# Kernel optimization log

Hardware: AMD Instinct MI355X
Metric: run time of the kernel (lower is better)

## Reference

```python
import jax, jax.numpy as jnp
import numpy as np

B, T, D_IN = 256, 250, 700
H1, H2, D_OUT = 256, 256, 20
B_J0 = 0.01
BETA = 1.8  # adaptation strength (isAdapt=1)
LENS, SCALE, HIGHT, GAMMA = 0.5, 6.0, 0.15, 0.5
SQRT_2PI = float(np.sqrt(2.0 * np.pi))


def _gaussian(x, mu, sigma):
    return jnp.exp(-((x - mu) ** 2) / (2.0 * sigma ** 2)) / (SQRT_2PI * sigma)


@jax.custom_vjp
def act_fun(x):
    # Heaviside spike with multi-Gaussian surrogate gradient (gradient_type='MG')
    return (x > 0).astype(x.dtype)


def _act_fwd(x):
    return act_fun(x), x


def _act_bwd(x, g):
    temp = (_gaussian(x, 0.0, LENS) * (1.0 + HIGHT)
            - _gaussian(x, LENS, SCALE * LENS) * HIGHT
            - _gaussian(x, -LENS, SCALE * LENS) * HIGHT)
    return (g * temp * GAMMA,)


act_fun.defvjp(_act_fwd, _act_bwd)


def setup_inputs() -> dict:
    key = jax.random.key(0)
    ks = jax.random.split(key, 16)
    # binary-ish spike input (SHD spike trains), rand fill
    x = (jax.random.uniform(ks[0], (B, T, D_IN)) < 0.1).astype(jnp.float32)

    def xavier(k, out_d, in_d):
        lim = float(np.sqrt(6.0 / (in_d + out_d)))
        return jax.random.uniform(k, (out_d, in_d), jnp.float32, -lim, lim)

    return {
        "x": x,
        "w_i2h1": xavier(ks[1], H1, D_IN),
        "w_h12h1": xavier(ks[2], H1, H1),
        "w_h12h2": xavier(ks[3], H2, H1),
        "w_h22h2": xavier(ks[4], H2, H2),
        "w_h2o": xavier(ks[5], D_OUT, H2),
        "b_h1": jnp.zeros((H1,), jnp.float32),
        "b_h2": jnp.zeros((H2,), jnp.float32),
        "b_o": jnp.zeros((D_OUT,), jnp.float32),
        "tau_adp_h1": 150.0 + 10.0 * jax.random.normal(ks[6], (H1,), jnp.float32),
        "tau_adp_h2": 150.0 + 10.0 * jax.random.normal(ks[7], (H2,), jnp.float32),
        "tau_m_h1": 20.0 + 5.0 * jax.random.normal(ks[8], (H1,), jnp.float32),
        "tau_m_h2": 20.0 + 5.0 * jax.random.normal(ks[9], (H2,), jnp.float32),
        "tau_m_o": 20.0 + 5.0 * jax.random.normal(ks[10], (D_OUT,), jnp.float32),
    }


def _lif_step(inp, mem, spk, b, alpha, ro):
    # mem_update_adp with params=None, dparams=None, isAdapt=1, dt=1, R_m=1
    b = ro * b + BETA * (1.0 - ro) * spk
    mem = mem * alpha - b * spk + (1.0 - alpha) * inp
    spk = act_fun(mem - b - B_J0)
    return mem, spk, b


def reference(x, w_i2h1, w_h12h1, w_h12h2, w_h22h2, w_h2o,
              b_h1, b_h2, b_o, tau_adp_h1, tau_adp_h2,
              tau_m_h1, tau_m_h2, tau_m_o):
    bsz = x.shape[0]
    h1, h2, d_out = w_i2h1.shape[0], w_h12h2.shape[0], w_h2o.shape[0]

    alpha1 = jnp.exp(-1.0 / tau_m_h1)
    ro1 = jnp.exp(-1.0 / tau_adp_h1)
    alpha2 = jnp.exp(-1.0 / tau_m_h2)
    ro2 = jnp.exp(-1.0 / tau_adp_h2)
    alpha_o = jnp.exp(-1.0 / tau_m_o)

    init = (
        jnp.zeros((bsz, h1)), jnp.zeros((bsz, h1)), jnp.full((bsz, h1), B_J0),
        jnp.zeros((bsz, h2)), jnp.zeros((bsz, h2)), jnp.full((bsz, h2), B_J0),
        jnp.zeros((bsz, d_out)), jnp.zeros((bsz, d_out)),
    )
    xT = jnp.swapaxes(x, 0, 1)  # [T, B, D_in]

    def step(carry, xt):
        mem1, spk1, bb1, mem2, spk2, bb2, mem_o, acc = carry
        h1_in = xt @ w_i2h1.T + spk1 @ w_h12h1.T + b_h1
        mem1, spk1, bb1 = _lif_step(h1_in, mem1, spk1, bb1, alpha1, ro1)
        h2_in = spk1 @ w_h12h2.T + spk2 @ w_h22h2.T + b_h2
        mem2, spk2, bb2 = _lif_step(h2_in, mem2, spk2, bb2, alpha2, ro2)
        o_in = spk2 @ w_h2o.T + b_o
        mem_o = mem_o * alpha_o + (1.0 - alpha_o) * o_in  # output_Neuron
        acc = acc + jax.nn.softmax(mem_o, axis=-1)
        return (mem1, spk1, bb1, mem2, spk2, bb2, mem_o, acc), None

    carry, _ = jax.lax.scan(step, init, xT)
    return carry[-1]  # accumulated softmax over the 250 timesteps, [B, 20]
```

## Files before the change

kernel.cpp:

```cpp
#include <hip/hip_runtime.h>
#include <cstdint>
#include <cstddef>

#define BB 256
#define TT 250
#define DIN 700
#define H1 256
#define H2 256
#define DOUT 20
#define BJ0 0.01f
#define BETAC 1.8f
#define DUMMY 256
#define IQSCALE 3.814697265625e-06f

typedef float f32x4 __attribute__((ext_vector_type(4)));
typedef short s16x4 __attribute__((ext_vector_type(4)));
typedef int   i32x4 __attribute__((ext_vector_type(4)));

#define COFF_BL  180224
#define IOFF_P12 90112
#define SOFF_T22 311808
#define FOFF_W2O 188800
#define FOFF_XP  193944
#define FOFF_MO  16577944
#define N_TRANS  316948

#define BARRIER_LDS() asm volatile("s_waitcnt lgkmcnt(0)\n\ts_barrier" ::: "memory")

__device__ __forceinline__ short q18(float w) {
    float s = w * 262144.0f;
    s = fminf(fmaxf(s, -32767.0f), 32767.0f);
    return (short)__float2int_rn(s);
}

__global__ void transpose_all_k(const float* __restrict__ w_i2h1,
                                const float* __restrict__ w_h12h1,
                                const float* __restrict__ w_h12h2,
                                const float* __restrict__ w_h22h2,
                                const float* __restrict__ w_h2o,
                                signed char* __restrict__ cws,
                                short* __restrict__ sws,
                                int* __restrict__ iws,
                                float* __restrict__ fws) {
    int i = blockIdx.x * blockDim.x + threadIdx.x;
    if (i < 180224) {
        int h = i / 704, k = i - h * 704;
        int q = (k < DIN) ? (int)q18(w_i2h1[h * DIN + k]) : 0;
        q = q > 32639 ? 32639 : (q < -32640 ? -32640 : q);
        int hi = (q + 128) >> 8;
        int lo = q - (hi << 8);
        cws[i] = (signed char)hi;
        cws[COFF_BL + i] = (signed char)lo;
        return;
    }
    i -= 180224;
    if (i < 65792) { int d = i >> 8, h = i & 255;
        unsigned int lo = 0, hi = 0;
        if (d < H1) {
            lo = (unsigned short)q18(w_h12h1[h * H1 + d]);
            hi = (unsigned short)q18(w_h12h2[h * H1 + d]);
        }
        iws[IOFF_P12 + i] = (int)(lo | (hi << 16)); return; }
    i -= 65792;
    if (i < 65792) { int d = i >> 8, h = i & 255;
        sws[SOFF_T22 + i] = q18((d < H2) ? w_h22h2[h * H2 + d] : 0.f); return; }
    i -= 65792;
    if (i < 5140)  { int j = i / 20, h = i % 20;
        fws[FOFF_W2O + i] = (j < H2) ? w_h2o[h * H2 + j] : 0.f; return; }
}

__global__ __launch_bounds__(256) void xgemm_k(const float* __restrict__ x,
                                               const signed char* __restrict__ Bh,
                                               const signed char* __restrict__ Bl,
                                               const float* __restrict__ b_h1,
                                               float* __restrict__ Xp) {
    const int t    = threadIdx.x;
    const int lane = t & 63;
    const int w    = t >> 6;
    const int m0   = blockIdx.x * 32;

    __shared__ __align__(16) signed char Asub[32 * 720];
    __shared__ __align__(16) signed char Bhs[256 * 80];
    __shared__ __align__(16) signed char Bls[256 * 80];

    #pragma unroll
    for (int it = 0; it < 22; ++it) {
        int flat = it * 256 + t;
        int row  = flat / 176;
        int c4   = flat - row * 176;
        unsigned int pk = 0u;
        if (c4 < 175) {
            const float* xr = x + (size_t)(m0 + row) * DIN;
            float4 f = *(const float4*)(xr + (c4 << 2));
            pk = (f.x != 0.f ? 1u : 0u)
               | (f.y != 0.f ? 1u : 0u) << 8
               | (f.z != 0.f ? 1u : 0u) << 16
               | (f.w != 0.f ? 1u : 0u) << 24;
        }
        *(unsigned int*)(Asub + row * 720 + (c4 << 2)) = pk;
    }

    i32x4 acch[2][4], accl[2][4];
    #pragma unroll
    for (int mt = 0; mt < 2; ++mt)
        #pragma unroll
        for (int nt = 0; nt < 4; ++nt) {
            acch[mt][nt] = (i32x4){0, 0, 0, 0};
            accl[mt][nt] = (i32x4){0, 0, 0, 0};
        }

    const int arow  = lane & 15;
    const int kg16  = (lane >> 4) << 4;
    const int bcol0 = w << 6;

    for (int ks = 0; ks < 11; ++ks) {
        __syncthreads();
        #pragma unroll
        for (int it2 = 0; it2 < 4; ++it2) {
            int row = it2 * 64 + (t >> 2);
            int ch  = (t & 3) << 4;
            int go  = row * 704 + ks * 64 + ch;
            *(int4*)(Bhs + row * 80 + ch) = *(const int4*)(Bh + go);
            *(int4*)(Bls + row * 80 + ch) = *(const int4*)(Bl + go);
        }
        __syncthreads();

        const int ko = ks * 64 + kg16;
        i32x4 a0 = *(const i32x4*)(Asub + arow * 720 + ko);
        i32x4 a1 = *(const i32x4*)(Asub + (16 + arow) * 720 + ko);
        #pragma unroll
        for (int nt = 0; nt < 4; ++nt) {
            const int bb = (bcol0 + nt * 16 + arow) * 80 + kg16;
            i32x4 bhf = *(const i32x4*)(Bhs + bb);
            i32x4 blf = *(const i32x4*)(Bls + bb);
            acch[0][nt] = __builtin_amdgcn_mfma_i32_16x16x64_i8(a0, bhf, acch[0][nt], 0, 0, 0);
            acch[1][nt] = __builtin_amdgcn_mfma_i32_16x16x64_i8(a1, bhf, acch[1][nt], 0, 0, 0);
            accl[0][nt] = __builtin_amdgcn_mfma_i32_16x16x64_i8(a0, blf, accl[0][nt], 0, 0, 0);
            accl[1][nt] = __builtin_amdgcn_mfma_i32_16x16x64_i8(a1, blf, accl[1][nt], 0, 0, 0);
        }
    }

    const int crb = (lane >> 4) << 2;
    #pragma unroll
    for (int nt = 0; nt < 4; ++nt) {
        int col = bcol0 + nt * 16 + arow;
        float bias = b_h1[col];
        #pragma unroll
        for (int mt = 0; mt < 2; ++mt) {
            #pragma unroll
            for (int r = 0; r < 4; ++r) {
                int row = m0 + mt * 16 + crb + r;
                int ir = (acch[mt][nt][r] << 8) + accl[mt][nt][r];
                __builtin_nontemporal_store(bias + (float)ir * IQSCALE,
                                            Xp + (size_t)row * H1 + col);
            }
        }
    }
}

__global__ __launch_bounds__(512) void rec_k(
    const float* __restrict__ Xp,
    const int*   __restrict__ sP12,
    const short* __restrict__ sT22, const float* __restrict__ wT2o,
    const float* __restrict__ b_h2, const float* __restrict__ b_o,
    const float* __restrict__ tau_adp_h1, const float* __restrict__ tau_adp_h2,
    const float* __restrict__ tau_m_h1, const float* __restrict__ tau_m_h2,
    const float* __restrict__ tau_m_o,
    float* __restrict__ Mo) {
    const int tid  = threadIdx.x;
    const int h    = tid & 255;
    const int half = tid >> 8;
    const int lane = tid & 63;
    const int g    = tid >> 6;
    const int l4   = lane << 2;
    const int b    = blockIdx.x;
    const float* __restrict__ XpB = Xp + (size_t)b * TT * H1;
    float* __restrict__ MoB = Mo + (size_t)b * TT * DOUT;

    __shared__ __align__(16) short sT22L[65792];
    __shared__ __align__(16) int lst1s[2][256];
    __shared__ __align__(16) int lst2s[2][256];
    __shared__ __align__(16) int lcnt[2][2];
    __shared__ __align__(16) int pp11[8][256];
    __shared__ __align__(16) int pp12[8][256];
    __shared__ __align__(16) int pp22[8][256];
    __shared__ __align__(16) float pro[8][20];

    {
        const int* src = (const int*)sT22;
        int* dst = (int*)sT22L;
        for (int i2 = tid; i2 < 32896; i2 += 512) dst[i2] = src[i2];
        if (tid < 4) lcnt[tid >> 1][tid & 1] = 0;
    }

    const float alpha1 = expf(-1.0f / tau_m_h1[h]);
    const float ro1    = expf(-1.0f / tau_adp_h1[h]);
    const float alpha2 = expf(-1.0f / tau_m_h2[h]);
    const float ro2    = expf(-1.0f / tau_adp_h2[h]);
    const float bh2v   = b_h2[h];
    float alpo = 0.f, bov = 0.f;
    if (h < DOUT) { alpo = expf(-1.0f / tau_m_o[h]); bov = b_o[h]; }

    float mem1 = 0.f, spk1 = 0.f, bb1v = BJ0;
    float mem2 = 0.f, spk2 = 0.f, bb2v = BJ0;
    float memo = 0.f;

    float xp_cur = 0.f;
    if (half == 0) xp_cur = __builtin_nontemporal_load(XpB + h);
    __syncthreads();

    for (int i = 0; i <= TT + 1; ++i) {
        const int cur = i & 1, nxt = cur ^ 1;

        float xp_nxt = 0.f;
        if (half == 0 && i + 1 < TT)
            xp_nxt = __builtin_nontemporal_load(XpB + (size_t)(i + 1) * H1 + h);

        const int tot1 = lcnt[cur][0];
        const int tot2 = lcnt[cur][1];
        const int n1p = (tot1 + 31) & ~31;
        const int n2p = (tot2 + 31) & ~31;

        if (half == 0) lst1s[nxt][h] = DUMMY; else lst2s[nxt][h] = DUMMY;
        if (tid == 0)   lcnt[nxt][0] = 0;
        if (tid == 256) lcnt[nxt][1] = 0;

        int a110 = 0, a111 = 0, a112 = 0, a113 = 0;
        int a120 = 0, a121 = 0, a122 = 0, a123 = 0;
        int a220 = 0, a221 = 0, a222 = 0, a223 = 0;
        float ao0 = 0.f, ao1 = 0.f, ao2 = 0.f, ao3 = 0.f;

        const int gbase = g << 5;
        const int ng1 = n1p >> 3;
        for (int kk = 0; kk < ng1; kk += 4) {
            int4 e = *(const int4*)&lst1s[cur][gbase + kk];
            int4 pa = *(const int4*)(sP12 + ((size_t)e.x << 8) + l4);
            int4 pb = *(const int4*)(sP12 + ((size_t)e.y << 8) + l4);
            int4 pc = *(const int4*)(sP12 + ((size_t)e.z << 8) + l4);
            int4 pd = *(const int4*)(sP12 + ((size_t)e.w << 8) + l4);
            a110 += ((int)(short)pa.x + (int)(short)pb.x) + ((int)(short)pc.x + (int)(short)pd.x);
            a111 += ((int)(short)pa.y + (int)(short)pb.y) + ((int)(short)pc.y + (int)(short)pd.y);
            a112 += ((int)(short)pa.z + (int)(short)pb.z) + ((int)(short)pc.z + (int)(short)pd.z);
            a113 += ((int)(short)pa.w + (int)(short)pb.w) + ((int)(short)pc.w + (int)(short)pd.w);
            a120 += ((pa.x >> 16) + (pb.x >> 16)) + ((pc.x >> 16) + (pd.x >> 16));
            a121 += ((pa.y >> 16) + (pb.y >> 16)) + ((pc.y >> 16) + (pd.y >> 16));
            a122 += ((pa.z >> 16) + (pb.z >> 16)) + ((pc.z >> 16) + (pd.z >> 16));
            a123 += ((pa.w >> 16) + (pb.w >> 16)) + ((pc.w >> 16) + (pd.w >> 16));
        }
        const int ng2 = n2p >> 3;
        for (int kk = 0; kk < ng2; kk += 4) {
            int4 e = *(const int4*)&lst2s[cur][gbase + kk];
            s16x4 wa = *(const s16x4*)(sT22L + (e.x << 8) + l4);
            s16x4 wb = *(const s16x4*)(sT22L + (e.y << 8) + l4);
            s16x4 wc = *(const s16x4*)(sT22L + (e.z << 8) + l4);
            s16x4 wd = *(const s16x4*)(sT22L + (e.w << 8) + l4);
            a220 += (wa.x + wb.x) + (wc.x + wd.x);
            a221 += (wa.y + wb.y) + (wc.y + wd.y);
            a222 += (wa.z + wb.z) + (wc.z + wd.z);
            a223 += (wa.w + wb.w) + (wc.w + wd.w);
            if (lane < 5) {
                float4 va = *(const float4*)(wT2o + e.x * DOUT + l4);
                float4 vb = *(const float4*)(wT2o + e.y * DOUT + l4);
                float4 vc = *(const float4*)(wT2o + e.z * DOUT + l4);
                float4 vd = *(const float4*)(wT2o + e.w * DOUT + l4);
                ao0 += (va.x + vb.x) + (vc.x + vd.x);
                ao1 += (va.y + vb.y) + (vc.y + vd.y);
                ao2 += (va.z + vb.z) + (vc.z + vd.z);
                ao3 += (va.w + vb.w) + (vc.w + vd.w);
            }
        }
        {
            int4 v;
            v.x = a110; v.y = a111; v.z = a112; v.w = a113;
            *(int4*)&pp11[g][l4] = v;
            v.x = a120; v.y = a121; v.z = a122; v.w = a123;
            *(int4*)&pp12[g][l4] = v;
            v.x = a220; v.y = a221; v.z = a222; v.w = a223;
            *(int4*)&pp22[g][l4] = v;
        }
        if (lane < 5) {
            float4 v; v.x = ao0; v.y = ao1; v.z = ao2; v.w = ao3;
            *(float4*)&pro[g][l4] = v;
        }
        BARRIER_LDS();

        if (half == 0) {
            if (i < TT) {
                int ir11 = ((pp11[0][h] + pp11[1][h]) + (pp11[2][h] + pp11[3][h]))
                         + ((pp11[4][h] + pp11[5][h]) + (pp11[6][h] + pp11[7][h]));
                float r1 = (float)ir11 * IQSCALE;
                bb1v = ro1 * bb1v + BETAC * (1.f - ro1) * spk1;
                mem1 = mem1 * alpha1 - bb1v * spk1 + (1.f - alpha1) * (xp_cur + r1);
                float ns1 = (mem1 - bb1v - BJ0) > 0.f ? 1.f : 0.f;
                spk1 = ns1;
                unsigned long long m1 = __ballot(ns1 != 0.f ? 1 : 0);
                int c = __popcll(m1);
                int base = 0;
                if (lane == 0) base = atomicAdd(&lcnt[nxt][0], c);
                base = __shfl(base, 0);
                if (ns1 != 0.f) {
                    int pos = base + __popcll(m1 & ((1ull << lane) - 1ull));
                    lst1s[nxt][((pos & 7) << 5) + (pos >> 3)] = h;
                }
            }
        } else {
            if (i >= 1 && i <= TT) {
                int ir12 = ((pp12[0][h] + pp12[1][h]) + (pp12[2][h] + pp12[3][h]))
                         + ((pp12[4][h] + pp12[5][h]) + (pp12[6][h] + pp12[7][h]));
                int ir22 = ((pp22[0][h] + pp22[1][h]) + (pp22[2][h] + pp22[3][h]))
                         + ((pp22[4][h] + pp22[5][h]) + (pp22[6][h] + pp22[7][h]));
                float r23 = (float)(ir22 + ir12) * IQSCALE;
                bb2v = ro2 * bb2v + BETAC * (1.f - ro2) * spk2;
                mem2 = mem2 * alpha2 - bb2v * spk2 + (1.f - alpha2) * (bh2v + r23);
                float ns2 = (mem2 - bb2v - BJ0) > 0.f ? 1.f : 0.f;
                spk2 = ns2;
                unsigned long long m2 = __ballot(ns2 != 0.f ? 1 : 0);
                int c = __popcll(m2);
                int base = 0;
                if (lane == 0) base = atomicAdd(&lcnt[nxt][1], c);
                base = __shfl(base, 0);
                if (ns2 != 0.f) {
                    int pos = base + __popcll(m2 & ((1ull << lane) - 1ull));
                    lst2s[nxt][((pos & 7) << 5) + (pos >> 3)] = h;
                }
            }
            if ((h < DOUT) && (i >= 2)) {
                float ro = ((pro[0][h] + pro[1][h]) + (pro[2][h] + pro[3][h]))
                         + ((pro[4][h] + pro[5][h]) + (pro[6][h] + pro[7][h]));
                memo = memo * alpo + (1.f - alpo) * (bov + ro);
                __builtin_nontemporal_store(memo, MoB + (size_t)(i - 2) * DOUT + h);
            }
        }
        BARRIER_LDS();

        xp_cur = xp_nxt;
    }
}

__global__ __launch_bounds__(256) void soft_k(const float* __restrict__ Mo,
                                              float* __restrict__ out) {
    const int b = blockIdx.x;
    const int t = threadIdx.x;
    __shared__ float sm[TT][DOUT];

    if (t < TT) {
        const float* row = Mo + ((size_t)b * TT + t) * DOUT;
        float v[DOUT];
        #pragma unroll
        for (int k = 0; k < DOUT; k += 4) {
            float4 r = *(const float4*)(row + k);
            v[k] = r.x; v[k + 1] = r.y; v[k + 2] = r.z; v[k + 3] = r.w;
        }
        float mx = v[0];
        #pragma unroll
        for (int j = 1; j < DOUT; ++j) mx = fmaxf(mx, v[j]);
        float s = 0.f;
        #pragma unroll
        for (int j = 0; j < DOUT; ++j) { v[j] = __expf(v[j] - mx); s += v[j]; }
        float inv = 1.0f / s;
        #pragma unroll
        for (int j = 0; j < DOUT; ++j) sm[t][j] = v[j] * inv;
    }
    __syncthreads();
    if (t < DOUT) {
        float acc = 0.f;
        for (int tt = 0; tt < TT; ++tt) acc += sm[tt][t];
        out[b * DOUT + t] = acc;
    }
}

extern "C" void kernel_launch(void* const* d_in, const int* in_sizes, int n_in,
                              void* d_out, int out_size, void* d_ws, size_t ws_size,
                              hipStream_t stream) {
    const float* x          = (const float*)d_in[0];
    const float* w_i2h1     = (const float*)d_in[1];
    const float* w_h12h1    = (const float*)d_in[2];
    const float* w_h12h2    = (const float*)d_in[3];
    const float* w_h22h2    = (const float*)d_in[4];
    const float* w_h2o      = (const float*)d_in[5];
    const float* b_h1       = (const float*)d_in[6];
    const float* b_h2       = (const float*)d_in[7];
    const float* b_o        = (const float*)d_in[8];
    const float* tau_adp_h1 = (const float*)d_in[9];
    const float* tau_adp_h2 = (const float*)d_in[10];
    const float* tau_m_h1   = (const float*)d_in[11];
    const float* tau_m_h2   = (const float*)d_in[12];
    const float* tau_m_o    = (const float*)d_in[13];

    signed char* cws = (signed char*)d_ws;
    short* sws = (short*)d_ws;
    int*   iws = (int*)d_ws;
    float* fws = (float*)d_ws;
    const signed char* Bh = cws;
    const signed char* Bl = cws + COFF_BL;
    const int*   sP12 = iws + IOFF_P12;
    const short* sT22 = sws + SOFF_T22;
    float* wT2o = fws + FOFF_W2O;
    float* Xp   = fws + FOFF_XP;
    float* Mo   = fws + FOFF_MO;

    transpose_all_k<<<(N_TRANS + 255) / 256, 256, 0, stream>>>(
        w_i2h1, w_h12h1, w_h12h2, w_h22h2, w_h2o, cws, sws, iws, fws);

    xgemm_k<<<(BB * TT) / 32, 256, 0, stream>>>(x, Bh, Bl, b_h1, Xp);

    rec_k<<<BB, 512, 0, stream>>>(Xp, sP12, sT22, wT2o,
                                  b_h2, b_o, tau_adp_h1, tau_adp_h2,
                                  tau_m_h1, tau_m_h2, tau_m_o, Mo);

    soft_k<<<BB, 256, 0, stream>>>(Mo, (float*)d_out);
}
```

Before: 753.8 us.

## Assign layer-1 and layer-2 neurons to separate waves with one barrier per step

Restructures the recurrent kernel so waves 0-3 own layer-1 neurons and waves 4-7 own layer-2 neurons. Each thread gathers its own column over the full spike list, instead of splitting the spike list across waves and reducing partial sums through shared memory. This removes the partial-sum arrays and one of the two barriers per timestep. The spike-count slots are now rotated over four entries, and the output weights are staged in LDS. In exchange each thread does serial gathers over the whole spike list, which lengthens the per-step critical path when many neurons spike. The split layer-1/layer-2 weight arrays also use scalar 16-bit gathers from global memory rather than packed vector loads.

Measured after the change: 689.6 us. -8.5%, faster.

```diff
diff --git a/kernel.cpp b/kernel.cpp
--- a/kernel.cpp
+++ b/kernel.cpp
@@ -10,20 +10,19 @@
 #define DOUT 20
 #define BJ0 0.01f
 #define BETAC 1.8f
-#define DUMMY 256
 #define IQSCALE 3.814697265625e-06f
 
 typedef float f32x4 __attribute__((ext_vector_type(4)));
-typedef short s16x4 __attribute__((ext_vector_type(4)));
 typedef int   i32x4 __attribute__((ext_vector_type(4)));
 
 #define COFF_BL  180224
-#define IOFF_P12 90112
-#define SOFF_T22 311808
-#define FOFF_W2O 188800
-#define FOFF_XP  193944
-#define FOFF_MO  16577944
-#define N_TRANS  316948
+#define SOFF_T11 180224
+#define SOFF_T12 245760
+#define SOFF_T22 311296
+#define FOFF_W2O 188416
+#define FOFF_XP  193536
+#define FOFF_MO  16577536
+#define N_TRANS  381952
 
 #define BARRIER_LDS() asm volatile("s_waitcnt lgkmcnt(0)\n\ts_barrier" ::: "memory")
 
@@ -40,7 +39,6 @@
                                 const float* __restrict__ w_h2o,
                                 signed char* __restrict__ cws,
                                 short* __restrict__ sws,
-                                int* __restrict__ iws,
                                 float* __restrict__ fws) {
     int i = blockIdx.x * blockDim.x + threadIdx.x;
     if (i < 180224) {
@@ -54,19 +52,17 @@
         return;
     }
     i -= 180224;
-    if (i < 65792) { int d = i >> 8, h = i & 255;
-        unsigned int lo = 0, hi = 0;
-        if (d < H1) {
-            lo = (unsigned short)q18(w_h12h1[h * H1 + d]);
-            hi = (unsigned short)q18(w_h12h2[h * H1 + d]);
-        }
-        iws[IOFF_P12 + i] = (int)(lo | (hi << 16)); return; }
-    i -= 65792;
-    if (i < 65792) { int d = i >> 8, h = i & 255;
-        sws[SOFF_T22 + i] = q18((d < H2) ? w_h22h2[h * H2 + d] : 0.f); return; }
-    i -= 65792;
-    if (i < 5140)  { int j = i / 20, h = i % 20;
-        fws[FOFF_W2O + i] = (j < H2) ? w_h2o[h * H2 + j] : 0.f; return; }
+    if (i < 65536) { int d = i >> 8, h = i & 255;
+        sws[SOFF_T11 + i] = q18(w_h12h1[h * H1 + d]); return; }
+    i -= 65536;
+    if (i < 65536) { int d = i >> 8, h = i & 255;
+        sws[SOFF_T12 + i] = q18(w_h12h2[h * H1 + d]); return; }
+    i -= 65536;
+    if (i < 65536) { int d = i >> 8, h = i & 255;
+        sws[SOFF_T22 + i] = q18(w_h22h2[h * H2 + d]); return; }
+    i -= 65536;
+    if (i < 5120)  { int j = i / 20, o = i % 20;
+        fws[FOFF_W2O + i] = w_h2o[o * H2 + j]; return; }
 }
 
 __global__ __launch_bounds__(256) void xgemm_k(const float* __restrict__ x,
@@ -160,7 +156,7 @@
 
 __global__ __launch_bounds__(512) void rec_k(
     const float* __restrict__ Xp,
-    const int*   __restrict__ sP12,
+    const short* __restrict__ sT11, const short* __restrict__ sT12,
     const short* __restrict__ sT22, const float* __restrict__ wT2o,
     const float* __restrict__ b_h2, const float* __restrict__ b_o,
     const float* __restrict__ tau_adp_h1, const float* __restrict__ tau_adp_h2,
@@ -168,171 +164,168 @@
     const float* __restrict__ tau_m_o,
     float* __restrict__ Mo) {
     const int tid  = threadIdx.x;
-    const int h    = tid & 255;
-    const int half = tid >> 8;
     const int lane = tid & 63;
-    const int g    = tid >> 6;
-    const int l4   = lane << 2;
+    const int w    = tid >> 6;
+    const bool isL1 = (w < 4);
+    const int c    = ((w & 3) << 6) + lane;
     const int b    = blockIdx.x;
     const float* __restrict__ XpB = Xp + (size_t)b * TT * H1;
     float* __restrict__ MoB = Mo + (size_t)b * TT * DOUT;
 
-    __shared__ __align__(16) short sT22L[65792];
+    __shared__ __align__(16) short sT22L[65536];
+    __shared__ __align__(16) float w2oL[5120];
     __shared__ __align__(16) int lst1s[2][256];
     __shared__ __align__(16) int lst2s[2][256];
-    __shared__ __align__(16) int lcnt[2][2];
-    __shared__ __align__(16) int pp11[8][256];
-    __shared__ __align__(16) int pp12[8][256];
-    __shared__ __align__(16) int pp22[8][256];
-    __shared__ __align__(16) float pro[8][20];
+    __shared__ __align__(16) int lcnt[4][2];
 
     {
         const int* src = (const int*)sT22;
         int* dst = (int*)sT22L;
-        for (int i2 = tid; i2 < 32896; i2 += 512) dst[i2] = src[i2];
-        if (tid < 4) lcnt[tid >> 1][tid & 1] = 0;
-    }
-
-    const float alpha1 = expf(-1.0f / tau_m_h1[h]);
-    const float ro1    = expf(-1.0f / tau_adp_h1[h]);
-    const float alpha2 = expf(-1.0f / tau_m_h2[h]);
-    const float ro2    = expf(-1.0f / tau_adp_h2[h]);
-    const float bh2v   = b_h2[h];
+        for (int k = tid; k < 32768; k += 512) dst[k] = src[k];
+        for (int k = tid; k < 5120; k += 512) w2oL[k] = wT2o[k];
+        if (tid < 256) { lst1s[0][tid] = 0; lst1s[1][tid] = 0;
+                         lst2s[0][tid] = 0; lst2s[1][tid] = 0; }
+        if (tid < 8) ((int*)lcnt)[tid] = 0;
+    }
+
+    float alpha, rr, inb = 0.f;
+    if (isL1) {
+        alpha = expf(-1.0f / tau_m_h1[c]);
+        rr    = expf(-1.0f / tau_adp_h1[c]);
+    } else {
+        alpha = expf(-1.0f / tau_m_h2[c]);
+        rr    = expf(-1.0f / tau_adp_h2[c]);
+        inb   = b_h2[c];
+    }
+    const int oc  = ((w & 3) * 5) + lane;
+    const int ocs = (isL1 && lane < 5) ? oc : 0;
     float alpo = 0.f, bov = 0.f;
-    if (h < DOUT) { alpo = expf(-1.0f / tau_m_o[h]); bov = b_o[h]; }
-
-    float mem1 = 0.f, spk1 = 0.f, bb1v = BJ0;
-    float mem2 = 0.f, spk2 = 0.f, bb2v = BJ0;
+    if (isL1 && lane < 5) { alpo = expf(-1.0f / tau_m_o[oc]); bov = b_o[oc]; }
+
+    float mem = 0.f, spk = 0.f, bbv = BJ0;
     float memo = 0.f;
 
     float xp_cur = 0.f;
-    if (half == 0) xp_cur = __builtin_nontemporal_load(XpB + h);
+    if (isL1) xp_cur = __builtin_nontemporal_load(XpB + c);
     __syncthreads();
 
     for (int i = 0; i <= TT + 1; ++i) {
         const int cur = i & 1, nxt = cur ^ 1;
+        const int cc = i & 3, cn = (i + 1) & 3, cz = (i + 2) & 3;
+
+        const int tot1 = lcnt[cc][0];
+        const int tot2 = lcnt[cc][1];
+        if (tid == 0) { lcnt[cz][0] = 0; lcnt[cz][1] = 0; }
 
         float xp_nxt = 0.f;
-        if (half == 0 && i + 1 < TT)
-            xp_nxt = __builtin_nontemporal_load(XpB + (size_t)(i + 1) * H1 + h);
-
-        const int tot1 = lcnt[cur][0];
-        const int tot2 = lcnt[cur][1];
-        const int n1p = (tot1 + 31) & ~31;
-        const int n2p = (tot2 + 31) & ~31;
-
-        if (half == 0) lst1s[nxt][h] = DUMMY; else lst2s[nxt][h] = DUMMY;
-        if (tid == 0)   lcnt[nxt][0] = 0;
-        if (tid == 256) lcnt[nxt][1] = 0;
-
-        int a110 = 0, a111 = 0, a112 = 0, a113 = 0;
-        int a120 = 0, a121 = 0, a122 = 0, a123 = 0;
-        int a220 = 0, a221 = 0, a222 = 0, a223 = 0;
-        float ao0 = 0.f, ao1 = 0.f, ao2 = 0.f, ao3 = 0.f;
-
-        const int gbase = g << 5;
-        const int ng1 = n1p >> 3;
-        for (int kk = 0; kk < ng1; kk += 4) {
-            int4 e = *(const int4*)&lst1s[cur][gbase + kk];
-            int4 pa = *(const int4*)(sP12 + ((size_t)e.x << 8) + l4);
-            int4 pb = *(const int4*)(sP12 + ((size_t)e.y << 8) + l4);
-            int4 pc = *(const int4*)(sP12 + ((size_t)e.z << 8) + l4);
-            int4 pd = *(const int4*)(sP12 + ((size_t)e.w << 8) + l4);
-            a110 += ((int)(short)pa.x + (int)(short)pb.x) + ((int)(short)pc.x + (int)(short)pd.x);
-            a111 += ((int)(short)pa.y + (int)(short)pb.y) + ((int)(short)pc.y + (int)(short)pd.y);
-            a112 += ((int)(short)pa.z + (int)(short)pb.z) + ((int)(short)pc.z + (int)(short)pd.z);
-            a113 += ((int)(short)pa.w + (int)(short)pb.w) + ((int)(short)pc.w + (int)(short)pd.w);
-            a120 += ((pa.x >> 16) + (pb.x >> 16)) + ((pc.x >> 16) + (pd.x >> 16));
-            a121 += ((pa.y >> 16) + (pb.y >> 16)) + ((pc.y >> 16) + (pd.y >> 16));
-            a122 += ((pa.z >> 16) + (pb.z >> 16)) + ((pc.z >> 16) + (pd.z >> 16));
-            a123 += ((pa.w >> 16) + (pb.w >> 16)) + ((pc.w >> 16) + (pd.w >> 16));
-        }
-        const int ng2 = n2p >> 3;
-        for (int kk = 0; kk < ng2; kk += 4) {
-            int4 e = *(const int4*)&lst2s[cur][gbase + kk];
-            s16x4 wa = *(const s16x4*)(sT22L + (e.x << 8) + l4);
-            s16x4 wb = *(const s16x4*)(sT22L + (e.y << 8) + l4);
-            s16x4 wc = *(const s16x4*)(sT22L + (e.z << 8) + l4);
-            s16x4 wd = *(const s16x4*)(sT22L + (e.w << 8) + l4);
-            a220 += (wa.x + wb.x) + (wc.x + wd.x);
-            a221 += (wa.y + wb.y) + (wc.y + wd.y);
-            a222 += (wa.z + wb.z) + (wc.z + wd.z);
-            a223 += (wa.w + wb.w) + (wc.w + wd.w);
-            if (lane < 5) {
-                float4 va = *(const float4*)(wT2o + e.x * DOUT + l4);
-                float4 vb = *(const float4*)(wT2o + e.y * DOUT + l4);
-                float4 vc = *(const float4*)(wT2o + e.z * DOUT + l4);
-                float4 vd = *(const float4*)(wT2o + e.w * DOUT + l4);
-                ao0 += (va.x + vb.x) + (vc.x + vd.x);
-                ao1 += (va.y + vb.y) + (vc.y + vd.y);
-                ao2 += (va.z + vb.z) + (vc.z + vd.z);
-                ao3 += (va.w + vb.w) + (vc.w + vd.w);
-            }
-        }
-        {
-            int4 v;
-            v.x = a110; v.y = a111; v.z = a112; v.w = a113;
-            *(int4*)&pp11[g][l4] = v;
-            v.x = a120; v.y = a121; v.z = a122; v.w = a123;
-            *(int4*)&pp12[g][l4] = v;
-            v.x = a220; v.y = a221; v.z = a222; v.w = a223;
-            *(int4*)&pp22[g][l4] = v;
-        }
-        if (lane < 5) {
-            float4 v; v.x = ao0; v.y = ao1; v.z = ao2; v.w = ao3;
-            *(float4*)&pro[g][l4] = v;
-        }
+        if (isL1 && i + 1 < TT)
+            xp_nxt = __builtin_nontemporal_load(XpB + (size_t)(i + 1) * H1 + c);
+
+        const int* __restrict__ L1l = lst1s[cur];
+        const int* __restrict__ L2l = lst2s[cur];
+
+        int acc1 = 0, acc2 = 0;
+        float ao = 0.f;
+
+        if (isL1) {
+            if (i < TT) {
+                const short* colT = sT11 + c;
+                int nb = tot1 >> 2, rem = tot1 & 3;
+                for (int kk = 0; kk < nb; ++kk) {
+                    int4 e = *(const int4*)(L1l + (kk << 2));
+                    acc1 += colT[e.x << 8]; acc1 += colT[e.y << 8];
+                    acc1 += colT[e.z << 8]; acc1 += colT[e.w << 8];
+                }
+                if (rem) {
+                    int4 e = *(const int4*)(L1l + (nb << 2));
+                    acc1 += colT[e.x << 8];
+                    if (rem > 1) acc1 += colT[e.y << 8];
+                    if (rem > 2) acc1 += colT[e.z << 8];
+                }
+            }
+            if (i >= 2) {
+                int nb = tot2 >> 2, rem = tot2 & 3;
+                for (int kk = 0; kk < nb; ++kk) {
+                    int4 e = *(const int4*)(L2l + (kk << 2));
+                    float v0 = w2oL[e.x * DOUT + ocs];
+                    float v1 = w2oL[e.y * DOUT + ocs];
+                    float v2 = w2oL[e.z * DOUT + ocs];
+                    float v3 = w2oL[e.w * DOUT + ocs];
+                    ao += (v0 + v1) + (v2 + v3);
+                }
+                if (rem) {
+                    int4 e = *(const int4*)(L2l + (nb << 2));
+                    ao += w2oL[e.x * DOUT + ocs];
+                    if (rem > 1) ao += w2oL[e.y * DOUT + ocs];
+                    if (rem > 2) ao += w2oL[e.z * DOUT + ocs];
+                }
+            }
+        } else if (i >= 1 && i <= TT) {
+            {
+                const short* colT = sT12 + c;
+                int nb = tot1 >> 2, rem = tot1 & 3;
+                for (int kk = 0; kk < nb; ++kk) {
+                    int4 e = *(const int4*)(L1l + (kk << 2));
+                    acc1 += colT[e.x << 8]; acc1 += colT[e.y << 8];
+                    acc1 += colT[e.z << 8]; acc1 += colT[e.w << 8];
+                }
+                if (rem) {
+                    int4 e = *(const int4*)(L1l + (nb << 2));
+                    acc1 += colT[e.x << 8];
+                    if (rem > 1) acc1 += colT[e.y << 8];
+                    if (rem > 2) acc1 += colT[e.z << 8];
+                }
+            }
+            {
+                const short* colL = sT22L + c;
+                int nb = tot2 >> 2, rem = tot2 & 3;
+                for (int kk = 0; kk < nb; ++kk) {
+                    int4 e = *(const int4*)(L2l + (kk << 2));
+                    acc2 += colL[e.x << 8]; acc2 += colL[e.y << 8];
+                    acc2 += colL[e.z << 8]; acc2 += colL[e.w << 8];
+                }
+                if (rem) {
+                    int4 e = *(const int4*)(L2l + (nb << 2));
+                    acc2 += colL[e.x << 8];
+                    if (rem > 1) acc2 += colL[e.y << 8];
+                    if (rem > 2) acc2 += colL[e.z << 8];
+                }
+            }
+        }
+
+        if (isL1) {
+            if (i < TT) {
+                float r1 = (float)acc1 * IQSCALE;
+                bbv = rr * bbv + BETAC * (1.f - rr) * spk;
+                mem = mem * alpha - bbv * spk + (1.f - alpha) * (xp_cur + r1);
+                float ns = (mem - bbv - BJ0) > 0.f ? 1.f : 0.f;
+                spk = ns;
+                unsigned long long m = __ballot(ns != 0.f ? 1 : 0);
+                int base = 0;
+                if (lane == 0) base = atomicAdd(&lcnt[cn][0], __popcll(m));
+                base = __shfl(base, 0);
+                if (ns != 0.f)
+                    lst1s[nxt][base + __popcll(m & ((1ull << lane) - 1ull))] = c;
+            }
+            if (lane < 5 && i >= 2) {
+                memo = memo * alpo + (1.f - alpo) * (bov + ao);
+                __builtin_nontemporal_store(memo, MoB + (size_t)(i - 2) * DOUT + oc);
+            }
+        } else if (i >= 1 && i <= TT) {
+            float r23 = (float)(acc1 + acc2) * IQSCALE;
+            bbv = rr * bbv + BETAC * (1.f - rr) * spk;
+            mem = mem * alpha - bbv * spk + (1.f - alpha) * (inb + r23);
+            float ns = (mem - bbv - BJ0) > 0.f ? 1.f : 0.f;
+            spk = ns;
+            unsigned long long m = __ballot(ns != 0.f ? 1 : 0);
+            int base = 0;
+            if (lane == 0) base = atomicAdd(&lcnt[cn][1], __popcll(m));
+            base = __shfl(base, 0);
+            if (ns != 0.f)
+                lst2s[nxt][base + __popcll(m & ((1ull << lane) - 1ull))] = c;
+        }
+
         BARRIER_LDS();
-
-        if (half == 0) {
-            if (i < TT) {
-                int ir11 = ((pp11[0][h] + pp11[1][h]) + (pp11[2][h] + pp11[3][h]))
-                         + ((pp11[4][h] + pp11[5][h]) + (pp11[6][h] + pp11[7][h]));
-                float r1 = (float)ir11 * IQSCALE;
-                bb1v = ro1 * bb1v + BETAC * (1.f - ro1) * spk1;
-                mem1 = mem1 * alpha1 - bb1v * spk1 + (1.f - alpha1) * (xp_cur + r1);
-                float ns1 = (mem1 - bb1v - BJ0) > 0.f ? 1.f : 0.f;
-                spk1 = ns1;
-                unsigned long long m1 = __ballot(ns1 != 0.f ? 1 : 0);
-                int c = __popcll(m1);
-                int base = 0;
-                if (lane == 0) base = atomicAdd(&lcnt[nxt][0], c);
-                base = __shfl(base, 0);
-                if (ns1 != 0.f) {
-                    int pos = base + __popcll(m1 & ((1ull << lane) - 1ull));
-                    lst1s[nxt][((pos & 7) << 5) + (pos >> 3)] = h;
-                }
-            }
-        } else {
-            if (i >= 1 && i <= TT) {
-                int ir12 = ((pp12[0][h] + pp12[1][h]) + (pp12[2][h] + pp12[3][h]))
-                         + ((pp12[4][h] + pp12[5][h]) + (pp12[6][h] + pp12[7][h]));
-                int ir22 = ((pp22[0][h] + pp22[1][h]) + (pp22[2][h] + pp22[3][h]))
-                         + ((pp22[4][h] + pp22[5][h]) + (pp22[6][h] + pp22[7][h]));
-                float r23 = (float)(ir22 + ir12) * IQSCALE;
-                bb2v = ro2 * bb2v + BETAC * (1.f - ro2) * spk2;
-                mem2 = mem2 * alpha2 - bb2v * spk2 + (1.f - alpha2) * (bh2v + r23);
-                float ns2 = (mem2 - bb2v - BJ0) > 0.f ? 1.f : 0.f;
-                spk2 = ns2;
-                unsigned long long m2 = __ballot(ns2 != 0.f ? 1 : 0);
-                int c = __popcll(m2);
-                int base = 0;
-                if (lane == 0) base = atomicAdd(&lcnt[nxt][1], c);
-                base = __shfl(base, 0);
-                if (ns2 != 0.f) {
-                    int pos = base + __popcll(m2 & ((1ull << lane) - 1ull));
-                    lst2s[nxt][((pos & 7) << 5) + (pos >> 3)] = h;
-                }
-            }
-            if ((h < DOUT) && (i >= 2)) {
-                float ro = ((pro[0][h] + pro[1][h]) + (pro[2][h] + pro[3][h]))
-                         + ((pro[4][h] + pro[5][h]) + (pro[6][h] + pro[7][h]));
-                memo = memo * alpo + (1.f - alpo) * (bov + ro);
-                __builtin_nontemporal_store(memo, MoB + (size_t)(i - 2) * DOUT + h);
-            }
-        }
-        BARRIER_LDS();
-
         xp_cur = xp_nxt;
     }
 }
@@ -389,22 +382,22 @@
 
     signed char* cws = (signed char*)d_ws;
     short* sws = (short*)d_ws;
-    int*   iws = (int*)d_ws;
     float* fws = (float*)d_ws;
     const signed char* Bh = cws;
     const signed char* Bl = cws + COFF_BL;
-    const int*   sP12 = iws + IOFF_P12;
+    const short* sT11 = sws + SOFF_T11;
+    const short* sT12 = sws + SOFF_T12;
     const short* sT22 = sws + SOFF_T22;
     float* wT2o = fws + FOFF_W2O;
     float* Xp   = fws + FOFF_XP;
     float* Mo   = fws + FOFF_MO;
 
-    transpose_all_k<<<(N_TRANS + 255) / 256, 256, 0, stream>>>(
-        w_i2h1, w_h12h1, w_h12h2, w_h22h2, w_h2o, cws, sws, iws, fws);
+    transpose_all_k<<<N_TRANS / 256, 256, 0, stream>>>(
+        w_i2h1, w_h12h1, w_h12h2, w_h22h2, w_h2o, cws, sws, fws);
 
     xgemm_k<<<(BB * TT) / 32, 256, 0, stream>>>(x, Bh, Bl, b_h1, Xp);
 
-    rec_k<<<BB, 512, 0, stream>>>(Xp, sP12, sT22, wT2o,
+    rec_k<<<BB, 512, 0, stream>>>(Xp, sT11, sT12, sT22, wT2o,
                                   b_h2, b_o, tau_adp_h1, tau_adp_h2,
                                   tau_m_h1, tau_m_h2, tau_m_o, Mo);
 
```
